# Performance work log

Measured on AMD Instinct MI355X. Metric: run time of the kernel, lower is better.

Reference implementation:

```python
import jax, jax.numpy as jnp
import numpy as np

D_MODEL = 256
D_FF = 1024
N_B = 4
LN_EPS = 1e-12


def setup_inputs() -> dict:
    key = jax.random.key(0)
    ks = jax.random.split(key, 8)
    B, T = 32, 2048
    x = jax.random.normal(ks[0], (B, T, D_MODEL), dtype=jnp.float32)
    b_seq = jax.random.randint(ks[1], (B, T), 0, N_B + 1, dtype=jnp.int32)
    # Per-behavior FFN params, stacked over branches (init std=0.02, zero bias)
    w1 = 0.02 * jax.random.normal(ks[2], (N_B, D_FF, D_MODEL), dtype=jnp.float32)
    b1 = jnp.zeros((N_B, D_FF), dtype=jnp.float32)
    w2 = 0.02 * jax.random.normal(ks[3], (N_B, D_MODEL, D_FF), dtype=jnp.float32)
    b2 = jnp.zeros((N_B, D_MODEL), dtype=jnp.float32)
    gamma = jnp.ones((N_B, D_MODEL), dtype=jnp.float32)
    beta = jnp.zeros((N_B, D_MODEL), dtype=jnp.float32)
    return {"x": x, "b_seq": b_seq, "w1": w1, "b1": b1, "w2": w2, "b2": b2, "gamma": gamma, "beta": beta}


def _layernorm(y, gamma, beta):
    # LN over last dim, eps=1e-12; gamma/beta broadcast over leading dims
    mu = jnp.mean(y, axis=-1, keepdims=True)
    var = jnp.mean((y - mu) ** 2, axis=-1, keepdims=True)
    return (y - mu) * jax.lax.rsqrt(var + LN_EPS) * gamma + beta


def reference(x, b_seq, w1, b1, w2, b2, gamma, beta):
    # x: [B,T,h]; run all n_b branch FFNs densely (faithful to original).
    h = jnp.einsum('bth,nfh->nbtf', x, w1) + b1[:, None, None, :]   # [n,B,T,f]
    h = jax.nn.elu(h)                                               # dropout is eval-mode identity
    y = jnp.einsum('nbtf,nhf->nbth', h, w2) + b2[:, None, None, :]  # [n,B,T,h]
    y = _layernorm(y, gamma[:, None, None, :], beta[:, None, None, :])
    # Prepend zeros branch (index 0), then one-hot select per token.
    stacked = jnp.concatenate([jnp.zeros_like(y[:1]), y], axis=0)   # [n+1,B,T,h]
    oh = jax.nn.one_hot(b_seq, N_B + 1, dtype=x.dtype)              # [B,T,n+1]
    return jnp.einsum('nbth,btn->bth', stacked, oh)
```

## Files before the change

### kernel.cpp

```cpp
#include <hip/hip_runtime.h>

#define TOK 65536
#define DM 256
#define DF 1024
#define NB 4

typedef unsigned short ushort_t;
typedef unsigned int uint32;

typedef __attribute__((ext_vector_type(8))) short bf16x8;
typedef __attribute__((ext_vector_type(4))) float f32x4;
typedef __attribute__((ext_vector_type(4))) uint32 u32x4;

__device__ inline ushort_t f2bf(float f) {
  union { float f; unsigned int u; } v; v.f = f;
  unsigned int u = v.u;
  unsigned int r = (u + 0x7FFFu + ((u >> 16) & 1u)) >> 16;
  return (ushort_t)r;
}
__device__ inline float bf2f(ushort_t u) {
  union { unsigned int u; float f; } v; v.u = ((uint32)u) << 16; return v.f;
}
__device__ inline uint32 pack2(float a, float b) {
  return (uint32)f2bf(a) | ((uint32)f2bf(b) << 16);
}

__device__ __forceinline__ void dma16(const ushort_t* g, ushort_t* lds) {
  __builtin_amdgcn_global_load_lds(
      (const __attribute__((address_space(1))) unsigned int*)(const void*)g,
      (__attribute__((address_space(3))) unsigned int*)(void*)lds,
      16, 0, 0);
}

__global__ __launch_bounds__(256) void prep_route_kernel(
    const float* __restrict__ w1, const float* __restrict__ w2,
    ushort_t* __restrict__ w1b, ushort_t* __restrict__ w2b,
    const int* __restrict__ b_seq, int* __restrict__ counts,
    ushort_t* __restrict__ lists, u32x4* __restrict__ out16)
{
  const int bx = blockIdx.x;
  const int tid = threadIdx.x;
  if (bx >= 256) {
    const int pb = bx - 256;
    const int idx = (pb & 1023) * 256 + tid;
    const float* src = (pb >> 10) ? w2 : w1;
    ushort_t* dst = (pb >> 10) ? w2b : w1b;
    f32x4 v = *(const f32x4*)(src + (size_t)idx * 4);
    uint2 p;
    p.x = pack2(v.x, v.y);
    p.y = pack2(v.z, v.w);
    *(uint2*)(dst + (size_t)idx * 4) = p;
    return;
  }
  __shared__ int s_lpos[NB];
  __shared__ int s_lbase[NB];
  __shared__ int s_b[256];
  const int base = bx * 256;
  const int token = base + tid;
  if (tid < NB) s_lpos[tid] = 0;
  __syncthreads();
  const int b = b_seq[token];
  s_b[tid] = b;
  int my = 0;
  if (b > 0) my = atomicAdd(&s_lpos[b - 1], 1);
  __syncthreads();
  if (tid < NB) s_lbase[tid] = atomicAdd(&counts[tid], s_lpos[tid]);
  __syncthreads();
  if (b > 0) lists[(b - 1) * TOK + s_lbase[b - 1] + my] = (ushort_t)token;
  const u32x4 z = (u32x4){0u, 0u, 0u, 0u};
  #pragma unroll 4
  for (int it = 0; it < 64; ++it) {
    int flat = it * 256 + tid;
    int tl = flat >> 6;
    int j = flat & 63;
    if (s_b[tl] == 0) out16[(size_t)(base + tl) * 64 + j] = z;
  }
}

__global__ __launch_bounds__(512, 4) void ffn_kernel(
    const float* __restrict__ x,
    const ushort_t* __restrict__ w1b_all, const float* __restrict__ b1,
    const ushort_t* __restrict__ w2b_all, const float* __restrict__ b2,
    const float* __restrict__ gamma, const float* __restrict__ beta,
    const int* __restrict__ counts, const ushort_t* __restrict__ lists,
    float* __restrict__ out)
{
  const int id = blockIdx.x;
  const int slot = id & 7;
  const int n = slot >> 1;
  const int tile = ((id >> 3) << 1) + (slot & 1);
  const int cnt = counts[n];
  const int tile0 = tile * 64;
  if (tile0 >= cnt) return;
  const int mvalid = min(64, cnt - tile0);

  __shared__ __align__(16) ushort_t sW1[2][8192];
  __shared__ __align__(16) ushort_t sW2[2][8192];
  __shared__ __align__(16) ushort_t sH[2][64][40];
  __shared__ ushort_t sB1[DF];
  __shared__ int s_idx[64];
  __shared__ float s_ps[4][64];
  __shared__ float s_pq[4][64];
  __shared__ float s_mu[64];
  __shared__ float s_rs[64];

  ushort_t (*sX)[256] = (ushort_t (*)[256])&sW1[0][0];

  const int tid  = threadIdx.x;
  const int wv   = tid >> 6;
  const int lane = tid & 63;
  const int q    = lane >> 4;
  const int lc   = lane & 15;
  const int fi   = wv & 1;
  const int mq   = wv >> 1;
  const int dq   = wv & 3;
  const int mh   = wv >> 2;

  const ushort_t* w1b = w1b_all + (size_t)n * DF * DM;
  const ushort_t* w2b = w2b_all + (size_t)n * DM * DF;

  if (tid < 64) {
    int i = tile0 + tid;
    s_idx[tid] = (int)lists[n * TOK + (i < cnt ? i : tile0)];
  }
  if (tid < 256) {
    f32x4 v = *(const f32x4*)(b1 + n * DF + tid * 4);
    uint2 p;
    p.x = pack2(v.x, v.y);
    p.y = pack2(v.z, v.w);
    *(uint2*)(sB1 + tid * 4) = p;
  }
  __syncthreads();

  #pragma unroll
  for (int it = 0; it < 4; ++it) {
    int flat = it * 512 + tid;
    int r = flat >> 5;
    int c8 = flat & 31;
    const float* xp = x + (size_t)s_idx[r] * DM + c8 * 8;
    f32x4 a = *(const f32x4*)xp;
    f32x4 c = *(const f32x4*)(xp + 4);
    u32x4 p;
    p.x = pack2(a.x, a.y); p.y = pack2(a.z, a.w);
    p.z = pack2(c.x, c.y); p.w = pack2(c.z, c.w);
    *(u32x4*)(&sX[r][(c8 ^ (r & 31)) * 8]) = p;
  }
  __syncthreads();

  bf16x8 xfrag[8];
  #pragma unroll
  for (int ks = 0; ks < 8; ++ks) {
    int row = mq * 16 + lc;
    int g = (ks * 4 + q) ^ (row & 31);
    xfrag[ks] = *(const bf16x8*)(&sX[row][g * 8]);
  }
  __syncthreads();

  auto issue_w1 = [&](int fc) {
    ushort_t* dst = sW1[fc & 1];
    const ushort_t* g1 = w1b + (size_t)(fc * 32) * DM;
    #pragma unroll
    for (int j = 0; j < 2; ++j) {
      int i = wv * 2 + j;
      int s = i * 64 + lane;
      int r1 = s >> 5, cp1 = s & 31;
      dma16(g1 + (size_t)r1 * DM + (size_t)(cp1 ^ r1) * 8, dst + i * 512);
    }
  };
  auto issue_w2 = [&](int fc) {
    ushort_t* dst = sW2[fc & 1];
    const ushort_t* g2 = w2b + fc * 32;
    #pragma unroll
    for (int j = 0; j < 2; ++j) {
      int i = wv * 2 + j;
      int s = i * 64 + lane;
      int d2 = s >> 2, cp2 = s & 3;
      int cps = cp2 ^ (d2 & 3) ^ ((d2 >> 2) & 3);
      dma16(g2 + (size_t)d2 * DF + (size_t)cps * 8, dst + i * 512);
    }
  };

  issue_w1(0);

  f32x4 yacc[2][4];
  #pragma unroll
  for (int mi2 = 0; mi2 < 2; ++mi2)
    #pragma unroll
    for (int di = 0; di < 4; ++di)
      yacc[mi2][di] = (f32x4){0.f, 0.f, 0.f, 0.f};

  const int r1row = fi * 16 + lc;
  const int cpw = (q ^ (lc & 3) ^ ((lc >> 2) & 3)) * 8;

  #pragma unroll 1
  for (int i = 0; i <= 32; ++i) {
    __builtin_amdgcn_sched_barrier(0);
    __builtin_amdgcn_s_waitcnt(0x0070);
    __builtin_amdgcn_s_barrier();
    __builtin_amdgcn_sched_barrier(0);

    if (i < 31) issue_w1(i + 1);
    if (i < 32) issue_w2(i);

    if (i < 32) {
      const ushort_t* w1row = sW1[i & 1] + r1row * 256;
      const float b1v = bf2f(sB1[i * 32 + fi * 16 + lc]);
      f32x4 ha = (f32x4){0.f, 0.f, 0.f, 0.f};
      f32x4 hb = (f32x4){0.f, 0.f, 0.f, 0.f};
      __builtin_amdgcn_s_setprio(1);
      #pragma unroll
      for (int ks = 0; ks < 4; ++ks) {
        int cpa = ((2 * ks) * 4 + q) ^ r1row;
        int cpb = ((2 * ks + 1) * 4 + q) ^ r1row;
        bf16x8 bfa = *(const bf16x8*)(w1row + cpa * 8);
        bf16x8 bfb = *(const bf16x8*)(w1row + cpb * 8);
        ha = __builtin_amdgcn_mfma_f32_16x16x32_bf16(xfrag[2 * ks],     bfa, ha, 0, 0, 0);
        hb = __builtin_amdgcn_mfma_f32_16x16x32_bf16(xfrag[2 * ks + 1], bfb, hb, 0, 0, 0);
      }
      __builtin_amdgcn_s_setprio(0);
      #pragma unroll
      for (int r4 = 0; r4 < 4; ++r4) {
        float v = ha[r4] + hb[r4] + b1v;
        v = (v > 0.f) ? v : (__expf(v) - 1.f);
        sH[i & 1][mq * 16 + q * 4 + r4][fi * 16 + lc] = f2bf(v);
      }
    }

    if (i >= 1) {
      const int rb = (i - 1) & 1;
      bf16x8 af[2];
      #pragma unroll
      for (int mi2 = 0; mi2 < 2; ++mi2)
        af[mi2] = *(const bf16x8*)(&sH[rb][mh * 32 + mi2 * 16 + lc][q * 8]);
      const ushort_t* w2base = &sW2[rb][0] + (size_t)(dq * 64 + lc) * 32 + cpw;
      __builtin_amdgcn_s_setprio(1);
      #pragma unroll
      for (int di = 0; di < 4; ++di) {
        bf16x8 bf = *(const bf16x8*)(w2base + di * 512);
        yacc[0][di] = __builtin_amdgcn_mfma_f32_16x16x32_bf16(af[0], bf, yacc[0][di], 0, 0, 0);
        yacc[1][di] = __builtin_amdgcn_mfma_f32_16x16x32_bf16(af[1], bf, yacc[1][di], 0, 0, 0);
      }
      __builtin_amdgcn_s_setprio(0);
    }
  }

  __syncthreads();
  float b2v[4], gv[4], bv[4];
  #pragma unroll
  for (int di = 0; di < 4; ++di) {
    int dcol = n * DM + dq * 64 + di * 16 + lc;
    b2v[di] = b2[dcol];
    gv[di]  = gamma[dcol];
    bv[di]  = beta[dcol];
  }
  #pragma unroll
  for (int mi2 = 0; mi2 < 2; ++mi2)
    #pragma unroll
    for (int di = 0; di < 4; ++di)
      #pragma unroll
      for (int r4 = 0; r4 < 4; ++r4)
        yacc[mi2][di][r4] += b2v[di];

  #pragma unroll
  for (int mi2 = 0; mi2 < 2; ++mi2) {
    #pragma unroll
    for (int r4 = 0; r4 < 4; ++r4) {
      float s = 0.f, sq = 0.f;
      #pragma unroll
      for (int di = 0; di < 4; ++di) {
        float v = yacc[mi2][di][r4];
        s += v; sq += v * v;
      }
      #pragma unroll
      for (int off = 1; off < 16; off <<= 1) {
        s  += __shfl_xor(s, off, 64);
        sq += __shfl_xor(sq, off, 64);
      }
      if (lc == 0) {
        int tok = mh * 32 + mi2 * 16 + q * 4 + r4;
        s_ps[dq][tok] = s;
        s_pq[dq][tok] = sq;
      }
    }
  }
  __syncthreads();
  if (tid < 64) {
    float s  = s_ps[0][tid] + s_ps[1][tid] + s_ps[2][tid] + s_ps[3][tid];
    float sq = s_pq[0][tid] + s_pq[1][tid] + s_pq[2][tid] + s_pq[3][tid];
    float mu = s * (1.f / 256.f);
    float var = fmaxf(sq * (1.f / 256.f) - mu * mu, 0.f);
    s_mu[tid] = mu;
    s_rs[tid] = rsqrtf(var + 1e-12f);
  }
  __syncthreads();

  #pragma unroll
  for (int mi2 = 0; mi2 < 2; ++mi2) {
    #pragma unroll
    for (int r4 = 0; r4 < 4; ++r4) {
      int tok = mh * 32 + mi2 * 16 + q * 4 + r4;
      if (tok < mvalid) {
        float mu = s_mu[tok], rs = s_rs[tok];
        size_t rowbase = (size_t)s_idx[tok] * DM + dq * 64;
        #pragma unroll
        for (int di = 0; di < 4; ++di) {
          float v = (yacc[mi2][di][r4] - mu) * rs * gv[di] + bv[di];
          out[rowbase + di * 16 + lc] = v;
        }
      }
    }
  }
}

extern "C" void kernel_launch(void* const* d_in, const int* in_sizes, int n_in,
                              void* d_out, int out_size, void* d_ws, size_t ws_size,
                              hipStream_t stream) {
  const float* x     = (const float*)d_in[0];
  const int*   b_seq = (const int*)d_in[1];
  const float* w1    = (const float*)d_in[2];
  const float* b1    = (const float*)d_in[3];
  const float* w2    = (const float*)d_in[4];
  const float* b2    = (const float*)d_in[5];
  const float* gamma = (const float*)d_in[6];
  const float* beta  = (const float*)d_in[7];
  float* out = (float*)d_out;

  int* counts = (int*)d_ws;
  ushort_t* lists = (ushort_t*)((char*)d_ws + 256);
  ushort_t* w1b = (ushort_t*)((char*)d_ws + 256 + 512 * 1024);
  ushort_t* w2b = w1b + (size_t)NB * DF * DM;

  hipMemsetAsync(counts, 0, 256, stream);
  hipLaunchKernelGGL(prep_route_kernel, dim3(2304), dim3(256), 0, stream,
                     w1, w2, w1b, w2b, b_seq, counts, lists, (u32x4*)d_out);
  hipLaunchKernelGGL(ffn_kernel, dim3(4096), dim3(512), 0, stream,
                     x, w1b, b1, w2b, b2, gamma, beta, counts, lists, out);
}
```

Baseline: 225.8 us.

## Pre-swizzle weights into MFMA fragment order and load directly to registers

The prep kernel now converts the FFN weights to bf16 in the exact per-lane MFMA fragment order, so the FFN kernel reads them from global/L2 straight into registers instead of staging them through LDS with global_load_lds. The FFN kernel shrinks to 256 threads and 32-token tiles with twice as many blocks, and uses a two-stage register double-buffer for the W2 fragments. This removes the LDS traffic and bank-conflict swizzling for the weights. In exchange every block re-reads the weights from cache with no LDS sharing between waves, and the smaller tiles halve weight reuse per block.

Measured after the change: 280.5 us. 24.2% more time.

```diff
diff --git a/kernel.cpp b/kernel.cpp
--- a/kernel.cpp
+++ b/kernel.cpp
@@ -25,31 +25,44 @@
   return (uint32)f2bf(a) | ((uint32)f2bf(b) << 16);
 }
 
-__device__ __forceinline__ void dma16(const ushort_t* g, ushort_t* lds) {
-  __builtin_amdgcn_global_load_lds(
-      (const __attribute__((address_space(1))) unsigned int*)(const void*)g,
-      (__attribute__((address_space(3))) unsigned int*)(void*)lds,
-      16, 0, 0);
+__device__ __forceinline__ void lbar() {
+  __builtin_amdgcn_sched_barrier(0);
+  __builtin_amdgcn_s_waitcnt(0xC07F);
+  __builtin_amdgcn_s_barrier();
+  __builtin_amdgcn_sched_barrier(0);
 }
 
 __global__ __launch_bounds__(256) void prep_route_kernel(
     const float* __restrict__ w1, const float* __restrict__ w2,
-    ushort_t* __restrict__ w1b, ushort_t* __restrict__ w2b,
+    ushort_t* __restrict__ w1fb, ushort_t* __restrict__ w2fb,
     const int* __restrict__ b_seq, int* __restrict__ counts,
     ushort_t* __restrict__ lists, u32x4* __restrict__ out16)
 {
   const int bx = blockIdx.x;
   const int tid = threadIdx.x;
   if (bx >= 256) {
-    const int pb = bx - 256;
-    const int idx = (pb & 1023) * 256 + tid;
-    const float* src = (pb >> 10) ? w2 : w1;
-    ushort_t* dst = (pb >> 10) ? w2b : w1b;
-    f32x4 v = *(const f32x4*)(src + (size_t)idx * 4);
-    uint2 p;
-    p.x = pack2(v.x, v.y);
-    p.y = pack2(v.z, v.w);
-    *(uint2*)(dst + (size_t)idx * 4) = p;
+    const bool isw2 = bx >= 768;
+    const int gid = (bx - (isw2 ? 768 : 256)) * 256 + tid;
+    const int lane_ = gid & 63;
+    const int lcq = lane_ & 15, qq = lane_ >> 4;
+    size_t src_off;
+    if (!isw2) {
+      int ks = (gid >> 6) & 7, fi = (gid >> 9) & 1;
+      int fc = (gid >> 10) & 31, nn = gid >> 15;
+      src_off = (size_t)(nn * 1024 + fc * 32 + fi * 16 + lcq) * 256 + ks * 32 + qq * 8;
+    } else {
+      int di = (gid >> 6) & 3, dqv = (gid >> 8) & 3;
+      int fc = (gid >> 10) & 31, nn = gid >> 15;
+      src_off = (size_t)(nn * 256 + dqv * 64 + di * 16 + lcq) * 1024 + fc * 32 + qq * 8;
+    }
+    const float* src = (isw2 ? w2 : w1) + src_off;
+    f32x4 a = *(const f32x4*)src;
+    f32x4 c = *(const f32x4*)(src + 4);
+    u32x4 p;
+    p.x = pack2(a.x, a.y); p.y = pack2(a.z, a.w);
+    p.z = pack2(c.x, c.y); p.w = pack2(c.z, c.w);
+    ushort_t* dst = isw2 ? w2fb : w1fb;
+    *(u32x4*)(dst + (size_t)gid * 8) = p;
     return;
   }
   __shared__ int s_lpos[NB];
@@ -77,10 +90,10 @@
   }
 }
 
-__global__ __launch_bounds__(512, 4) void ffn_kernel(
+__global__ __launch_bounds__(256, 3) void ffn_kernel(
     const float* __restrict__ x,
-    const ushort_t* __restrict__ w1b_all, const float* __restrict__ b1,
-    const ushort_t* __restrict__ w2b_all, const float* __restrict__ b2,
+    const ushort_t* __restrict__ w1f_all, const float* __restrict__ b1,
+    const ushort_t* __restrict__ w2f_all, const float* __restrict__ b2,
     const float* __restrict__ gamma, const float* __restrict__ beta,
     const int* __restrict__ counts, const ushort_t* __restrict__ lists,
     float* __restrict__ out)
@@ -90,21 +103,18 @@
   const int n = slot >> 1;
   const int tile = ((id >> 3) << 1) + (slot & 1);
   const int cnt = counts[n];
-  const int tile0 = tile * 64;
+  const int tile0 = tile * 32;
   if (tile0 >= cnt) return;
-  const int mvalid = min(64, cnt - tile0);
-
-  __shared__ __align__(16) ushort_t sW1[2][8192];
-  __shared__ __align__(16) ushort_t sW2[2][8192];
-  __shared__ __align__(16) ushort_t sH[2][64][40];
+  const int mvalid = min(32, cnt - tile0);
+
+  __shared__ __align__(16) ushort_t sX[32][256];
+  __shared__ __align__(16) ushort_t sH[2][32][40];
   __shared__ ushort_t sB1[DF];
-  __shared__ int s_idx[64];
-  __shared__ float s_ps[4][64];
-  __shared__ float s_pq[4][64];
-  __shared__ float s_mu[64];
-  __shared__ float s_rs[64];
-
-  ushort_t (*sX)[256] = (ushort_t (*)[256])&sW1[0][0];
+  __shared__ int s_idx[32];
+  __shared__ float s_ps[4][32];
+  __shared__ float s_pq[4][32];
+  __shared__ float s_mu[32];
+  __shared__ float s_rs[32];
 
   const int tid  = threadIdx.x;
   const int wv   = tid >> 6;
@@ -112,18 +122,17 @@
   const int q    = lane >> 4;
   const int lc   = lane & 15;
   const int fi   = wv & 1;
-  const int mq   = wv >> 1;
-  const int dq   = wv & 3;
-  const int mh   = wv >> 2;
-
-  const ushort_t* w1b = w1b_all + (size_t)n * DF * DM;
-  const ushort_t* w2b = w2b_all + (size_t)n * DM * DF;
-
-  if (tid < 64) {
+  const int mh   = wv >> 1;
+  const int dq   = wv;
+
+  const ushort_t* w1f = w1f_all + (size_t)n * 262144;
+  const ushort_t* w2f = w2f_all + (size_t)n * 262144;
+
+  if (tid < 32) {
     int i = tile0 + tid;
     s_idx[tid] = (int)lists[n * TOK + (i < cnt ? i : tile0)];
   }
-  if (tid < 256) {
+  {
     f32x4 v = *(const f32x4*)(b1 + n * DF + tid * 4);
     uint2 p;
     p.x = pack2(v.x, v.y);
@@ -134,7 +143,7 @@
 
   #pragma unroll
   for (int it = 0; it < 4; ++it) {
-    int flat = it * 512 + tid;
+    int flat = it * 256 + tid;
     int r = flat >> 5;
     int c8 = flat & 31;
     const float* xp = x + (size_t)s_idx[r] * DM + c8 * 8;
@@ -143,44 +152,17 @@
     u32x4 p;
     p.x = pack2(a.x, a.y); p.y = pack2(a.z, a.w);
     p.z = pack2(c.x, c.y); p.w = pack2(c.z, c.w);
-    *(u32x4*)(&sX[r][(c8 ^ (r & 31)) * 8]) = p;
+    *(u32x4*)(&sX[r][(c8 ^ r) * 8]) = p;
   }
   __syncthreads();
 
   bf16x8 xfrag[8];
   #pragma unroll
   for (int ks = 0; ks < 8; ++ks) {
-    int row = mq * 16 + lc;
-    int g = (ks * 4 + q) ^ (row & 31);
+    int row = mh * 16 + lc;
+    int g = (ks * 4 + q) ^ row;
     xfrag[ks] = *(const bf16x8*)(&sX[row][g * 8]);
   }
-  __syncthreads();
-
-  auto issue_w1 = [&](int fc) {
-    ushort_t* dst = sW1[fc & 1];
-    const ushort_t* g1 = w1b + (size_t)(fc * 32) * DM;
-    #pragma unroll
-    for (int j = 0; j < 2; ++j) {
-      int i = wv * 2 + j;
-      int s = i * 64 + lane;
-      int r1 = s >> 5, cp1 = s & 31;
-      dma16(g1 + (size_t)r1 * DM + (size_t)(cp1 ^ r1) * 8, dst + i * 512);
-    }
-  };
-  auto issue_w2 = [&](int fc) {
-    ushort_t* dst = sW2[fc & 1];
-    const ushort_t* g2 = w2b + fc * 32;
-    #pragma unroll
-    for (int j = 0; j < 2; ++j) {
-      int i = wv * 2 + j;
-      int s = i * 64 + lane;
-      int d2 = s >> 2, cp2 = s & 3;
-      int cps = cp2 ^ (d2 & 3) ^ ((d2 >> 2) & 3);
-      dma16(g2 + (size_t)d2 * DF + (size_t)cps * 8, dst + i * 512);
-    }
-  };
-
-  issue_w1(0);
 
   f32x4 yacc[2][4];
   #pragma unroll
@@ -189,62 +171,62 @@
     for (int di = 0; di < 4; ++di)
       yacc[mi2][di] = (f32x4){0.f, 0.f, 0.f, 0.f};
 
-  const int r1row = fi * 16 + lc;
-  const int cpw = (q ^ (lc & 3) ^ ((lc >> 2) & 3)) * 8;
-
+  bf16x8 w2A[4], w2B[4];
+
+  auto g2_load = [&](int fc, bf16x8 (&w2r)[4]) {
+    const ushort_t* p = w2f + (size_t)(fc * 4 + dq) * 2048 + lane * 8;
+    #pragma unroll
+    for (int di = 0; di < 4; ++di)
+      w2r[di] = *(const bf16x8*)(p + di * 512);
+  };
+  auto g2_comp = [&](int fc, bf16x8 (&w2r)[4]) {
+    const int rb = fc & 1;
+    bf16x8 af0 = *(const bf16x8*)(&sH[rb][lc][q * 8]);
+    bf16x8 af1 = *(const bf16x8*)(&sH[rb][16 + lc][q * 8]);
+    __builtin_amdgcn_s_setprio(1);
+    #pragma unroll
+    for (int di = 0; di < 4; ++di) {
+      yacc[0][di] = __builtin_amdgcn_mfma_f32_16x16x32_bf16(af0, w2r[di], yacc[0][di], 0, 0, 0);
+      yacc[1][di] = __builtin_amdgcn_mfma_f32_16x16x32_bf16(af1, w2r[di], yacc[1][di], 0, 0, 0);
+    }
+    __builtin_amdgcn_s_setprio(0);
+  };
+  auto g1 = [&](int fc) {
+    const ushort_t* p = w1f + (size_t)(fc * 2 + fi) * 4096 + lane * 8;
+    const float b1v = bf2f(sB1[fc * 32 + fi * 16 + lc]);
+    f32x4 ha = (f32x4){0.f, 0.f, 0.f, 0.f};
+    f32x4 hb = (f32x4){0.f, 0.f, 0.f, 0.f};
+    __builtin_amdgcn_s_setprio(1);
+    #pragma unroll
+    for (int k2 = 0; k2 < 4; ++k2) {
+      bf16x8 ba = *(const bf16x8*)(p + (2 * k2) * 512);
+      bf16x8 bb = *(const bf16x8*)(p + (2 * k2 + 1) * 512);
+      ha = __builtin_amdgcn_mfma_f32_16x16x32_bf16(xfrag[2 * k2],     ba, ha, 0, 0, 0);
+      hb = __builtin_amdgcn_mfma_f32_16x16x32_bf16(xfrag[2 * k2 + 1], bb, hb, 0, 0, 0);
+    }
+    __builtin_amdgcn_s_setprio(0);
+    #pragma unroll
+    for (int r4 = 0; r4 < 4; ++r4) {
+      float v = ha[r4] + hb[r4] + b1v;
+      v = (v > 0.f) ? v : (__expf(v) - 1.f);
+      sH[fc & 1][mh * 16 + q * 4 + r4][fi * 16 + lc] = f2bf(v);
+    }
+  };
+
+  g2_load(0, w2A);
+  g1(0);
   #pragma unroll 1
-  for (int i = 0; i <= 32; ++i) {
-    __builtin_amdgcn_sched_barrier(0);
-    __builtin_amdgcn_s_waitcnt(0x0070);
-    __builtin_amdgcn_s_barrier();
-    __builtin_amdgcn_sched_barrier(0);
-
-    if (i < 31) issue_w1(i + 1);
-    if (i < 32) issue_w2(i);
-
-    if (i < 32) {
-      const ushort_t* w1row = sW1[i & 1] + r1row * 256;
-      const float b1v = bf2f(sB1[i * 32 + fi * 16 + lc]);
-      f32x4 ha = (f32x4){0.f, 0.f, 0.f, 0.f};
-      f32x4 hb = (f32x4){0.f, 0.f, 0.f, 0.f};
-      __builtin_amdgcn_s_setprio(1);
-      #pragma unroll
-      for (int ks = 0; ks < 4; ++ks) {
-        int cpa = ((2 * ks) * 4 + q) ^ r1row;
-        int cpb = ((2 * ks + 1) * 4 + q) ^ r1row;
-        bf16x8 bfa = *(const bf16x8*)(w1row + cpa * 8);
-        bf16x8 bfb = *(const bf16x8*)(w1row + cpb * 8);
-        ha = __builtin_amdgcn_mfma_f32_16x16x32_bf16(xfrag[2 * ks],     bfa, ha, 0, 0, 0);
-        hb = __builtin_amdgcn_mfma_f32_16x16x32_bf16(xfrag[2 * ks + 1], bfb, hb, 0, 0, 0);
-      }
-      __builtin_amdgcn_s_setprio(0);
-      #pragma unroll
-      for (int r4 = 0; r4 < 4; ++r4) {
-        float v = ha[r4] + hb[r4] + b1v;
-        v = (v > 0.f) ? v : (__expf(v) - 1.f);
-        sH[i & 1][mq * 16 + q * 4 + r4][fi * 16 + lc] = f2bf(v);
-      }
-    }
-
-    if (i >= 1) {
-      const int rb = (i - 1) & 1;
-      bf16x8 af[2];
-      #pragma unroll
-      for (int mi2 = 0; mi2 < 2; ++mi2)
-        af[mi2] = *(const bf16x8*)(&sH[rb][mh * 32 + mi2 * 16 + lc][q * 8]);
-      const ushort_t* w2base = &sW2[rb][0] + (size_t)(dq * 64 + lc) * 32 + cpw;
-      __builtin_amdgcn_s_setprio(1);
-      #pragma unroll
-      for (int di = 0; di < 4; ++di) {
-        bf16x8 bf = *(const bf16x8*)(w2base + di * 512);
-        yacc[0][di] = __builtin_amdgcn_mfma_f32_16x16x32_bf16(af[0], bf, yacc[0][di], 0, 0, 0);
-        yacc[1][di] = __builtin_amdgcn_mfma_f32_16x16x32_bf16(af[1], bf, yacc[1][di], 0, 0, 0);
-      }
-      __builtin_amdgcn_s_setprio(0);
-    }
-  }
-
-  __syncthreads();
+  for (int i = 1; i < 32; i += 2) {
+    lbar();
+    g2_load(i, w2B);
+    g2_comp(i - 1, w2A);
+    g1(i);
+    lbar();
+    if (i + 1 < 32) g2_load(i + 1, w2A);
+    g2_comp(i, w2B);
+    if (i + 1 < 32) g1(i + 1);
+  }
+
   float b2v[4], gv[4], bv[4];
   #pragma unroll
   for (int di = 0; di < 4; ++di) {
@@ -277,14 +259,14 @@
         sq += __shfl_xor(sq, off, 64);
       }
       if (lc == 0) {
-        int tok = mh * 32 + mi2 * 16 + q * 4 + r4;
+        int tok = mi2 * 16 + q * 4 + r4;
         s_ps[dq][tok] = s;
         s_pq[dq][tok] = sq;
       }
     }
   }
   __syncthreads();
-  if (tid < 64) {
+  if (tid < 32) {
     float s  = s_ps[0][tid] + s_ps[1][tid] + s_ps[2][tid] + s_ps[3][tid];
     float sq = s_pq[0][tid] + s_pq[1][tid] + s_pq[2][tid] + s_pq[3][tid];
     float mu = s * (1.f / 256.f);
@@ -298,7 +280,7 @@
   for (int mi2 = 0; mi2 < 2; ++mi2) {
     #pragma unroll
     for (int r4 = 0; r4 < 4; ++r4) {
-      int tok = mh * 32 + mi2 * 16 + q * 4 + r4;
+      int tok = mi2 * 16 + q * 4 + r4;
       if (tok < mvalid) {
         float mu = s_mu[tok], rs = s_rs[tok];
         size_t rowbase = (size_t)s_idx[tok] * DM + dq * 64;
@@ -327,12 +309,12 @@
 
   int* counts = (int*)d_ws;
   ushort_t* lists = (ushort_t*)((char*)d_ws + 256);
-  ushort_t* w1b = (ushort_t*)((char*)d_ws + 256 + 512 * 1024);
-  ushort_t* w2b = w1b + (size_t)NB * DF * DM;
+  ushort_t* w1fb = (ushort_t*)((char*)d_ws + 256 + 512 * 1024);
+  ushort_t* w2fb = w1fb + (size_t)NB * DF * DM;
 
   hipMemsetAsync(counts, 0, 256, stream);
-  hipLaunchKernelGGL(prep_route_kernel, dim3(2304), dim3(256), 0, stream,
-                     w1, w2, w1b, w2b, b_seq, counts, lists, (u32x4*)d_out);
-  hipLaunchKernelGGL(ffn_kernel, dim3(4096), dim3(512), 0, stream,
-                     x, w1b, b1, w2b, b2, gamma, beta, counts, lists, out);
-}
+  hipLaunchKernelGGL(prep_route_kernel, dim3(1280), dim3(256), 0, stream,
+                     w1, w2, w1fb, w2fb, b_seq, counts, lists, (u32x4*)d_out);
+  hipLaunchKernelGGL(ffn_kernel, dim3(8192), dim3(256), 0, stream,
+                     x, w1fb, b1, w2fb, b2, gamma, beta, counts, lists, out);
+}
```

## Pre-swizzle W2 into MFMA fragment order and load it directly to registers

Applied to the files above, without the earlier changes.

The prep kernel now rewrites W2 into a bf16 layout that matches the per-lane MFMA B-fragment order. The FFN kernel then loads W2 straight from global memory into registers instead of staging it through double-buffered LDS. The main loop is unrolled by two with ping-pong register buffers, so the next chunk's W2 load overlaps the current compute. This frees 32KB of LDS and removes the LDS reads for W2, in exchange for more VGPRs and global-load latency that must be hidden within one step.

Result: slower. 296.7 us (+31.4%).

```diff
diff --git a/kernel.cpp b/kernel.cpp
--- a/kernel.cpp
+++ b/kernel.cpp
@@ -34,22 +34,35 @@
 
 __global__ __launch_bounds__(256) void prep_route_kernel(
     const float* __restrict__ w1, const float* __restrict__ w2,
-    ushort_t* __restrict__ w1b, ushort_t* __restrict__ w2b,
+    ushort_t* __restrict__ w1b, ushort_t* __restrict__ w2fb,
     const int* __restrict__ b_seq, int* __restrict__ counts,
     ushort_t* __restrict__ lists, u32x4* __restrict__ out16)
 {
   const int bx = blockIdx.x;
   const int tid = threadIdx.x;
+  if (bx >= 1280) {
+    const int gid = (bx - 1280) * 256 + tid;
+    const int lane_ = gid & 63;
+    const int lcq = lane_ & 15, qq = lane_ >> 4;
+    int di = (gid >> 6) & 3, dqv = (gid >> 8) & 3;
+    int fc = (gid >> 10) & 31, nn = gid >> 15;
+    size_t src_off = (size_t)(nn * 256 + dqv * 64 + di * 16 + lcq) * 1024 + fc * 32 + qq * 8;
+    const float* src = w2 + src_off;
+    f32x4 a = *(const f32x4*)src;
+    f32x4 c = *(const f32x4*)(src + 4);
+    u32x4 p;
+    p.x = pack2(a.x, a.y); p.y = pack2(a.z, a.w);
+    p.z = pack2(c.x, c.y); p.w = pack2(c.z, c.w);
+    *(u32x4*)(w2fb + (size_t)gid * 8) = p;
+    return;
+  }
   if (bx >= 256) {
-    const int pb = bx - 256;
-    const int idx = (pb & 1023) * 256 + tid;
-    const float* src = (pb >> 10) ? w2 : w1;
-    ushort_t* dst = (pb >> 10) ? w2b : w1b;
-    f32x4 v = *(const f32x4*)(src + (size_t)idx * 4);
+    const int idx = (bx - 256) * 256 + tid;
+    f32x4 v = *(const f32x4*)(w1 + (size_t)idx * 4);
     uint2 p;
     p.x = pack2(v.x, v.y);
     p.y = pack2(v.z, v.w);
-    *(uint2*)(dst + (size_t)idx * 4) = p;
+    *(uint2*)(w1b + (size_t)idx * 4) = p;
     return;
   }
   __shared__ int s_lpos[NB];
@@ -80,7 +93,7 @@
 __global__ __launch_bounds__(512, 4) void ffn_kernel(
     const float* __restrict__ x,
     const ushort_t* __restrict__ w1b_all, const float* __restrict__ b1,
-    const ushort_t* __restrict__ w2b_all, const float* __restrict__ b2,
+    const ushort_t* __restrict__ w2f_all, const float* __restrict__ b2,
     const float* __restrict__ gamma, const float* __restrict__ beta,
     const int* __restrict__ counts, const ushort_t* __restrict__ lists,
     float* __restrict__ out)
@@ -95,7 +108,6 @@
   const int mvalid = min(64, cnt - tile0);
 
   __shared__ __align__(16) ushort_t sW1[2][8192];
-  __shared__ __align__(16) ushort_t sW2[2][8192];
   __shared__ __align__(16) ushort_t sH[2][64][40];
   __shared__ ushort_t sB1[DF];
   __shared__ int s_idx[64];
@@ -117,7 +129,7 @@
   const int mh   = wv >> 2;
 
   const ushort_t* w1b = w1b_all + (size_t)n * DF * DM;
-  const ushort_t* w2b = w2b_all + (size_t)n * DM * DF;
+  const ushort_t* w2f = w2f_all + (size_t)n * 262144;
 
   if (tid < 64) {
     int i = tile0 + tid;
@@ -158,29 +170,21 @@
 
   auto issue_w1 = [&](int fc) {
     ushort_t* dst = sW1[fc & 1];
-    const ushort_t* g1 = w1b + (size_t)(fc * 32) * DM;
+    const ushort_t* g1p = w1b + (size_t)(fc * 32) * DM;
     #pragma unroll
     for (int j = 0; j < 2; ++j) {
       int i = wv * 2 + j;
       int s = i * 64 + lane;
       int r1 = s >> 5, cp1 = s & 31;
-      dma16(g1 + (size_t)r1 * DM + (size_t)(cp1 ^ r1) * 8, dst + i * 512);
-    }
-  };
-  auto issue_w2 = [&](int fc) {
-    ushort_t* dst = sW2[fc & 1];
-    const ushort_t* g2 = w2b + fc * 32;
-    #pragma unroll
-    for (int j = 0; j < 2; ++j) {
-      int i = wv * 2 + j;
-      int s = i * 64 + lane;
-      int d2 = s >> 2, cp2 = s & 3;
-      int cps = cp2 ^ (d2 & 3) ^ ((d2 >> 2) & 3);
-      dma16(g2 + (size_t)d2 * DF + (size_t)cps * 8, dst + i * 512);
-    }
-  };
-
-  issue_w1(0);
+      dma16(g1p + (size_t)r1 * DM + (size_t)(cp1 ^ r1) * 8, dst + i * 512);
+    }
+  };
+  auto w2load = [&](int fc, bf16x8 (&w2r)[4]) {
+    const ushort_t* p = w2f + (size_t)(fc * 4 + dq) * 2048 + lane * 8;
+    #pragma unroll
+    for (int di = 0; di < 4; ++di)
+      w2r[di] = *(const bf16x8*)(p + di * 512);
+  };
 
   f32x4 yacc[2][4];
   #pragma unroll
@@ -190,58 +194,68 @@
       yacc[mi2][di] = (f32x4){0.f, 0.f, 0.f, 0.f};
 
   const int r1row = fi * 16 + lc;
-  const int cpw = (q ^ (lc & 3) ^ ((lc >> 2) & 3)) * 8;
-
-  #pragma unroll 1
-  for (int i = 0; i <= 32; ++i) {
+
+  auto ebar = [&]() {
     __builtin_amdgcn_sched_barrier(0);
     __builtin_amdgcn_s_waitcnt(0x0070);
     __builtin_amdgcn_s_barrier();
     __builtin_amdgcn_sched_barrier(0);
-
+  };
+  auto g1 = [&](int fc) {
+    const ushort_t* w1row = sW1[fc & 1] + r1row * 256;
+    const float b1v = bf2f(sB1[fc * 32 + fi * 16 + lc]);
+    f32x4 ha = (f32x4){0.f, 0.f, 0.f, 0.f};
+    f32x4 hb = (f32x4){0.f, 0.f, 0.f, 0.f};
+    __builtin_amdgcn_s_setprio(1);
+    #pragma unroll
+    for (int ks = 0; ks < 4; ++ks) {
+      int cpa = ((2 * ks) * 4 + q) ^ r1row;
+      int cpb = ((2 * ks + 1) * 4 + q) ^ r1row;
+      bf16x8 bfa = *(const bf16x8*)(w1row + cpa * 8);
+      bf16x8 bfb = *(const bf16x8*)(w1row + cpb * 8);
+      ha = __builtin_amdgcn_mfma_f32_16x16x32_bf16(xfrag[2 * ks],     bfa, ha, 0, 0, 0);
+      hb = __builtin_amdgcn_mfma_f32_16x16x32_bf16(xfrag[2 * ks + 1], bfb, hb, 0, 0, 0);
+    }
+    __builtin_amdgcn_s_setprio(0);
+    #pragma unroll
+    for (int r4 = 0; r4 < 4; ++r4) {
+      float v = ha[r4] + hb[r4] + b1v;
+      v = (v > 0.f) ? v : (__expf(v) - 1.f);
+      sH[fc & 1][mq * 16 + q * 4 + r4][fi * 16 + lc] = f2bf(v);
+    }
+  };
+  auto g2_comp = [&](int fc, bf16x8 (&w2r)[4]) {
+    const int rb = fc & 1;
+    bf16x8 af0 = *(const bf16x8*)(&sH[rb][mh * 32 + lc][q * 8]);
+    bf16x8 af1 = *(const bf16x8*)(&sH[rb][mh * 32 + 16 + lc][q * 8]);
+    __builtin_amdgcn_s_setprio(1);
+    #pragma unroll
+    for (int di = 0; di < 4; ++di) {
+      yacc[0][di] = __builtin_amdgcn_mfma_f32_16x16x32_bf16(af0, w2r[di], yacc[0][di], 0, 0, 0);
+      yacc[1][di] = __builtin_amdgcn_mfma_f32_16x16x32_bf16(af1, w2r[di], yacc[1][di], 0, 0, 0);
+    }
+    __builtin_amdgcn_s_setprio(0);
+  };
+
+  bf16x8 w2A[4], w2B[4];
+
+  issue_w1(0);
+  ebar();
+  issue_w1(1);
+  w2load(0, w2A);
+  g1(0);
+  #pragma unroll 1
+  for (int i = 1; i < 32; i += 2) {
+    ebar();
     if (i < 31) issue_w1(i + 1);
-    if (i < 32) issue_w2(i);
-
-    if (i < 32) {
-      const ushort_t* w1row = sW1[i & 1] + r1row * 256;
-      const float b1v = bf2f(sB1[i * 32 + fi * 16 + lc]);
-      f32x4 ha = (f32x4){0.f, 0.f, 0.f, 0.f};
-      f32x4 hb = (f32x4){0.f, 0.f, 0.f, 0.f};
-      __builtin_amdgcn_s_setprio(1);
-      #pragma unroll
-      for (int ks = 0; ks < 4; ++ks) {
-        int cpa = ((2 * ks) * 4 + q) ^ r1row;
-        int cpb = ((2 * ks + 1) * 4 + q) ^ r1row;
-        bf16x8 bfa = *(const bf16x8*)(w1row + cpa * 8);
-        bf16x8 bfb = *(const bf16x8*)(w1row + cpb * 8);
-        ha = __builtin_amdgcn_mfma_f32_16x16x32_bf16(xfrag[2 * ks],     bfa, ha, 0, 0, 0);
-        hb = __builtin_amdgcn_mfma_f32_16x16x32_bf16(xfrag[2 * ks + 1], bfb, hb, 0, 0, 0);
-      }
-      __builtin_amdgcn_s_setprio(0);
-      #pragma unroll
-      for (int r4 = 0; r4 < 4; ++r4) {
-        float v = ha[r4] + hb[r4] + b1v;
-        v = (v > 0.f) ? v : (__expf(v) - 1.f);
-        sH[i & 1][mq * 16 + q * 4 + r4][fi * 16 + lc] = f2bf(v);
-      }
-    }
-
-    if (i >= 1) {
-      const int rb = (i - 1) & 1;
-      bf16x8 af[2];
-      #pragma unroll
-      for (int mi2 = 0; mi2 < 2; ++mi2)
-        af[mi2] = *(const bf16x8*)(&sH[rb][mh * 32 + mi2 * 16 + lc][q * 8]);
-      const ushort_t* w2base = &sW2[rb][0] + (size_t)(dq * 64 + lc) * 32 + cpw;
-      __builtin_amdgcn_s_setprio(1);
-      #pragma unroll
-      for (int di = 0; di < 4; ++di) {
-        bf16x8 bf = *(const bf16x8*)(w2base + di * 512);
-        yacc[0][di] = __builtin_amdgcn_mfma_f32_16x16x32_bf16(af[0], bf, yacc[0][di], 0, 0, 0);
-        yacc[1][di] = __builtin_amdgcn_mfma_f32_16x16x32_bf16(af[1], bf, yacc[1][di], 0, 0, 0);
-      }
-      __builtin_amdgcn_s_setprio(0);
-    }
+    w2load(i, w2B);
+    g1(i);
+    g2_comp(i - 1, w2A);
+    ebar();
+    if (i < 30) issue_w1(i + 2);
+    if (i + 1 < 32) w2load(i + 1, w2A);
+    if (i + 1 < 32) g1(i + 1);
+    g2_comp(i, w2B);
   }
 
   __syncthreads();
@@ -328,11 +342,11 @@
   int* counts = (int*)d_ws;
   ushort_t* lists = (ushort_t*)((char*)d_ws + 256);
   ushort_t* w1b = (ushort_t*)((char*)d_ws + 256 + 512 * 1024);
-  ushort_t* w2b = w1b + (size_t)NB * DF * DM;
+  ushort_t* w2fb = w1b + (size_t)NB * DF * DM;
 
   hipMemsetAsync(counts, 0, 256, stream);
-  hipLaunchKernelGGL(prep_route_kernel, dim3(2304), dim3(256), 0, stream,
-                     w1, w2, w1b, w2b, b_seq, counts, lists, (u32x4*)d_out);
+  hipLaunchKernelGGL(prep_route_kernel, dim3(1792), dim3(256), 0, stream,
+                     w1, w2, w1b, w2fb, b_seq, counts, lists, (u32x4*)d_out);
   hipLaunchKernelGGL(ffn_kernel, dim3(4096), dim3(512), 0, stream,
-                     x, w1b, b1, w2b, b2, gamma, beta, counts, lists, out);
-}
+                     x, w1b, b1, w2fb, b2, gamma, beta, counts, lists, out);
+}
```
